# Performance work log

Hardware: AMD Instinct MI355X
Metric: run time of the kernel (lower is better)

Reference implementation:

```python
import jax, jax.numpy as jnp
import numpy as np

RATIO = 4   # compression ratio (group size)
H = 6       # index heads
D = 64      # index head dim = max(8, 768//6//2)
TOPK = 8    # index_topk
EPS = 1e-6  # rms_norm eps


def rms_norm(x):
    return x * jax.lax.rsqrt(jnp.mean(jnp.square(x), axis=-1, keepdims=True) + EPS)


def setup_inputs() -> dict:
    key = jax.random.key(0)
    k1, k2, k3, k4, k5 = jax.random.split(key, 5)
    B, T, E = 4, 4096, 768
    s = 0.02
    return {
        "x": jax.random.normal(k1, (B, T, E), jnp.float32),
        "wq": jax.random.normal(k2, (E, H * D), jnp.float32) * s,
        "wk": jax.random.normal(k3, (E, H * D), jnp.float32) * s,
        "wg": jax.random.normal(k4, (E, H * D), jnp.float32) * s,
        "ape": jax.random.normal(k5, (RATIO, H, D), jnp.float32) * s,
    }


def reference(x, wq, wk, wg, ape):
    B, T, E = x.shape
    G = -(-T // RATIO)          # ceil(T / ratio)
    pad = G * RATIO - T

    # --- compress keys: gated pooling over ratio-groups ---
    k = (x @ wk).reshape(B, T, H, D)
    gate = (x @ wg).reshape(B, T, H, D)
    if pad:
        k = jnp.pad(k, ((0, 0), (0, pad), (0, 0), (0, 0)))
        gate = jnp.pad(gate, ((0, 0), (0, pad), (0, 0), (0, 0)), constant_values=-jnp.inf)
    k = k.reshape(B, G, RATIO, H, D)
    gate = gate.reshape(B, G, RATIO, H, D) + ape[None, None]
    w = jax.nn.softmax(gate.astype(jnp.float32), axis=2).astype(k.dtype)
    keys = rms_norm(jnp.sum(k * w, axis=2))           # [B,G,H,D]
    group_ends = jnp.minimum(jnp.arange(RATIO - 1, G * RATIO, RATIO), T - 1)  # [G]

    # --- query-key scores ---
    q = rms_norm((x @ wq).reshape(B, T, H, D))
    scores = jnp.einsum('bthd,bghd->bhtg', q, keys) * (D ** -0.5)
    scores = jnp.mean(scores, axis=1)                 # [B,T,G]

    # --- causal mask over group ends, then top-k selection ---
    causal = group_ends[None, None, :] <= jnp.arange(T)[None, :, None]  # [1,T,G]
    scores = jnp.where(causal, scores, -jnp.inf)
    topk = min(TOPK, G)
    _, sel = jax.lax.top_k(scores, topk)              # [B,T,topk]

    # scatter selected indices into boolean mask
    bi = jnp.arange(B)[:, None, None]
    ti = jnp.arange(T)[None, :, None]
    mask = jnp.zeros((B, T, G), dtype=bool).at[bi, ti, sel].set(True)
    return (mask & causal, group_ends)
```

## Files before the change

### kernel.cpp

```cpp
#include <hip/hip_runtime.h>
#include <hip/hip_bf16.h>
#include <math.h>

#define B_    4
#define T_    4096
#define E_    768
#define H_    6
#define D_    64
#define HD_   384
#define G_    1024
#define RATIO_ 4
#define TOPK_ 8
#define MT_   (B_*T_)
#define NS_   1152

typedef __attribute__((ext_vector_type(8))) short short8;
typedef __attribute__((ext_vector_type(4))) float f32x4;
typedef __hip_bfloat16 bf16;

#define GLD16(g, l) __builtin_amdgcn_global_load_lds( \
    (const __attribute__((address_space(1))) void*)(g), \
    (__attribute__((address_space(3))) void*)(l), 16, 0, 0)

static __device__ __forceinline__ unsigned short f2bf(float f) {
  bf16 h = __float2bfloat16(f);
  return __builtin_bit_cast(unsigned short, h);
}
static __device__ __forceinline__ unsigned umax_(unsigned a, unsigned b) { return a > b ? a : b; }
static __device__ __forceinline__ unsigned umin_(unsigned a, unsigned b) { return a > b ? b : a; }

__global__ __launch_bounds__(256) void cvt_x_kernel(
    const float* __restrict__ in, bf16* __restrict__ out)
{
  size_t i = (size_t)blockIdx.x * 256 + threadIdx.x;
  const float4* p = reinterpret_cast<const float4*>(in) + i * 2;
  float4 v0 = p[0], v1 = p[1];
  float f[8] = {v0.x, v0.y, v0.z, v0.w, v1.x, v1.y, v1.z, v1.w};
  union { unsigned short u[8]; short8 v; } r;
#pragma unroll
  for (int k = 0; k < 8; ++k) r.u[k] = f2bf(f[k]);
  *reinterpret_cast<short8*>(out + i * 8) = r.v;
}

__global__ __launch_bounds__(256) void cvt_w_t(
    const float* __restrict__ wq, const float* __restrict__ wk,
    const float* __restrict__ wg, bf16* __restrict__ outbase)
{
  const int z = blockIdx.z;
  const float* src = z == 0 ? wq : (z == 1 ? wk : wg);
  __shared__ float t[32][33];
  int r = threadIdx.x >> 5, c = threadIdx.x & 31;
  int k0 = blockIdx.x * 32, n0 = blockIdx.y * 32;
#pragma unroll
  for (int i = 0; i < 4; ++i)
    t[r + i * 8][c] = src[(size_t)(k0 + r + i * 8) * HD_ + n0 + c];
  __syncthreads();
#pragma unroll
  for (int i = 0; i < 4; ++i) {
    int cc = n0 + r + i * 8;
    int ro = (z == 0) ? cc : 384 + ((cc >> 4) << 5) + ((z - 1) << 4) + (cc & 15);
    outbase[(size_t)ro * E_ + k0 + c] = __float2bfloat16(t[c][r + i * 8]);
  }
}

__global__ __launch_bounds__(256, 3) void gemm_qkg_mfma(
    const bf16* __restrict__ X, const bf16* __restrict__ Ws,
    const float* __restrict__ ape, bf16* __restrict__ Q,
    bf16* __restrict__ keys)
{
  __shared__ bf16 lds[2][8192];
  const int tid = threadIdx.x;
  const int lane = tid & 63, wv = tid >> 6;
  const int ll = lane & 15, lh = lane >> 4;
  const int m0 = blockIdx.x * 128, n0 = blockIdx.y * 128;
  const int srow = tid >> 3;
  const int sslot = (((tid & 7) ^ ((tid >> 3) & 7)) << 3);
  const bf16* pS = Ws + (size_t)(n0 + srow) * E_ + sslot;
  const bf16* pA0 = X + (size_t)(m0 + wv * 32 + ll) * E_ + lh * 8;
  const bf16* pA1 = pA0 + (size_t)16 * E_;

#define STAGE(b, k0) do { \
    char* base_ = (char*)&lds[b][0] + tid * 16; \
    GLD16(pS + (k0),            base_); \
    GLD16(pS + 32 * E_ + (k0),  base_ + 4096); \
    GLD16(pS + 64 * E_ + (k0),  base_ + 8192); \
    GLD16(pS + 96 * E_ + (k0),  base_ + 12288); \
  } while (0)
#define LOAD_A(dst, k0) do { \
    dst[0][0] = *reinterpret_cast<const short8*>(pA0 + (k0)); \
    dst[0][1] = *reinterpret_cast<const short8*>(pA0 + (k0) + 32); \
    dst[1][0] = *reinterpret_cast<const short8*>(pA1 + (k0)); \
    dst[1][1] = *reinterpret_cast<const short8*>(pA1 + (k0) + 32); \
  } while (0)

  f32x4 acc[2][8];
#pragma unroll
  for (int m = 0; m < 2; ++m)
#pragma unroll
    for (int n = 0; n < 8; ++n) acc[m][n] = (f32x4){0.f, 0.f, 0.f, 0.f};

  short8 curA[2][2], nxtA[2][2];
  LOAD_A(curA, 0);
  STAGE(0, 0);
#pragma unroll
  for (int m = 0; m < 2; ++m)
#pragma unroll
    for (int s = 0; s < 2; ++s) nxtA[m][s] = curA[m][s];

#pragma unroll
  for (int k = 0; k < 12; ++k) {
    const int k0 = k * 64;
    if (k < 11) {
      LOAD_A(nxtA, k0 + 64);
      STAGE((k + 1) & 1, k0 + 64);
    }
    if (k < 11) asm volatile("s_waitcnt vmcnt(8)" ::: "memory");
    else        asm volatile("s_waitcnt vmcnt(0)" ::: "memory");
    __builtin_amdgcn_s_barrier();
    __builtin_amdgcn_sched_barrier(0);
    const bf16* Lb = &lds[k & 1][0];
    short8 b0[8];
#pragma unroll
    for (int n = 0; n < 8; ++n)
      b0[n] = *reinterpret_cast<const short8*>(
          &Lb[(n * 16 + ll) * 64 + ((lh ^ (ll & 7)) << 3)]);
    asm volatile("s_waitcnt lgkmcnt(0)" ::: "memory");
    __builtin_amdgcn_sched_barrier(0);
#pragma unroll
    for (int m = 0; m < 2; ++m)
#pragma unroll
      for (int n = 0; n < 8; ++n)
        acc[m][n] = __builtin_amdgcn_mfma_f32_16x16x32_bf16(curA[m][0], b0[n], acc[m][n], 0, 0, 0);
    short8 b1[8];
#pragma unroll
    for (int n = 0; n < 8; ++n)
      b1[n] = *reinterpret_cast<const short8*>(
          &Lb[(n * 16 + ll) * 64 + (((4 + lh) ^ (ll & 7)) << 3)]);
    asm volatile("s_waitcnt lgkmcnt(0)" ::: "memory");
    __builtin_amdgcn_sched_barrier(0);
    __builtin_amdgcn_s_barrier();
#pragma unroll
    for (int m = 0; m < 2; ++m)
#pragma unroll
      for (int n = 0; n < 8; ++n)
        acc[m][n] = __builtin_amdgcn_mfma_f32_16x16x32_bf16(curA[m][1], b1[n], acc[m][n], 0, 0, 0);
#pragma unroll
    for (int m = 0; m < 2; ++m)
#pragma unroll
      for (int s = 0; s < 2; ++s) curA[m][s] = nxtA[m][s];
  }
#undef STAGE
#undef LOAD_A

  if (blockIdx.y < 3) {
#pragma unroll
    for (int m = 0; m < 2; ++m)
#pragma unroll
      for (int j = 0; j < 4; ++j) {
        int row = m0 + wv * 32 + m * 16 + lh * 4 + j;
#pragma unroll
        for (int h = 0; h < 2; ++h) {
          float ss = 0.f;
#pragma unroll
          for (int n = 4 * h; n < 4 * h + 4; ++n) ss += acc[m][n][j] * acc[m][n][j];
          ss += __shfl_xor(ss, 1, 64); ss += __shfl_xor(ss, 2, 64);
          ss += __shfl_xor(ss, 4, 64); ss += __shfl_xor(ss, 8, 64);
          float scl = rsqrtf(ss * (1.0f / D_) + 1e-6f);
#pragma unroll
          for (int n = 4 * h; n < 4 * h + 4; ++n)
            Q[(size_t)row * HD_ + n0 + n * 16 + ll] =
                __float2bfloat16(acc[m][n][j] * scl);
        }
      }
  } else {
    const int hcb = (n0 - 384) >> 1;
    float apev[4][4];
#pragma unroll
    for (int p = 0; p < 4; ++p) {
      int hc = hcb + p * 16 + ll;
#pragma unroll
      for (int j = 0; j < 4; ++j) apev[p][j] = ape[j * HD_ + hc];
    }
#pragma unroll
    for (int m = 0; m < 2; ++m) {
      float pooled[4];
#pragma unroll
      for (int p = 0; p < 4; ++p) {
        float g0 = acc[m][2 * p + 1][0] + apev[p][0];
        float g1 = acc[m][2 * p + 1][1] + apev[p][1];
        float g2 = acc[m][2 * p + 1][2] + apev[p][2];
        float g3 = acc[m][2 * p + 1][3] + apev[p][3];
        float mx = fmaxf(fmaxf(g0, g1), fmaxf(g2, g3));
        float e0 = expf(g0 - mx), e1 = expf(g1 - mx);
        float e2 = expf(g2 - mx), e3 = expf(g3 - mx);
        float inv = 1.0f / (e0 + e1 + e2 + e3);
        pooled[p] = (acc[m][2 * p][0] * e0 + acc[m][2 * p][1] * e1 +
                     acc[m][2 * p][2] * e2 + acc[m][2 * p][3] * e3) * inv;
      }
      float ss = pooled[0] * pooled[0] + pooled[1] * pooled[1] +
                 pooled[2] * pooled[2] + pooled[3] * pooled[3];
      ss += __shfl_xor(ss, 1, 64); ss += __shfl_xor(ss, 2, 64);
      ss += __shfl_xor(ss, 4, 64); ss += __shfl_xor(ss, 8, 64);
      float scl = rsqrtf(ss * (1.0f / D_) + 1e-6f);
      int prow = (m0 >> 2) + wv * 8 + m * 4 + lh;
#pragma unroll
      for (int p = 0; p < 4; ++p)
        keys[(size_t)prow * HD_ + hcb + p * 16 + ll] =
            __float2bfloat16(pooled[p] * scl);
    }
  }
}

#define CEx(a, bb) { unsigned h_ = umax_(a, bb), l_ = umin_(a, bb); a = h_; bb = l_; }
#define MERGE4() \
  _Pragma("unroll") \
  for (int st = 0; st < 2; ++st) { \
    const int off = 16 << st; \
    unsigned p0 = (unsigned)__shfl_xor((int)v0, off, 64); \
    unsigned p1 = (unsigned)__shfl_xor((int)v1, off, 64); \
    unsigned p2 = (unsigned)__shfl_xor((int)v2, off, 64); \
    unsigned p3 = (unsigned)__shfl_xor((int)v3, off, 64); \
    unsigned p4 = (unsigned)__shfl_xor((int)v4, off, 64); \
    unsigned p5 = (unsigned)__shfl_xor((int)v5, off, 64); \
    unsigned p6 = (unsigned)__shfl_xor((int)v6, off, 64); \
    unsigned p7 = (unsigned)__shfl_xor((int)v7, off, 64); \
    unsigned w0 = umax_(v0, p7), w1 = umax_(v1, p6); \
    unsigned w2 = umax_(v2, p5), w3 = umax_(v3, p4); \
    unsigned w4 = umax_(v4, p3), w5 = umax_(v5, p2); \
    unsigned w6 = umax_(v6, p1), w7 = umax_(v7, p0); \
    CEx(w0, w4); CEx(w1, w5); CEx(w2, w6); CEx(w3, w7); \
    CEx(w0, w2); CEx(w1, w3); CEx(w4, w6); CEx(w5, w7); \
    CEx(w0, w1); CEx(w2, w3); CEx(w4, w5); CEx(w6, w7); \
    v0 = w0; v1 = w1; v2 = w2; v3 = w3; v4 = w4; v5 = w5; v6 = w6; v7 = w7; \
  }

__global__ __launch_bounds__(128, 2) void score_topk8(
    const bf16* __restrict__ Qall, const bf16* __restrict__ Kall,
    int* __restrict__ mask, int* __restrict__ ends)
{
  __shared__ bf16 kbuf[2][12288];
  const int x = blockIdx.x;
  const int b = blockIdx.y;
  const int s = (b < 2) ? x : 127 - x;
  const int R0 = s << 5;
  const int tid = threadIdx.x;
  const int w = tid >> 6;
  const int lane = tid & 63;
  const int ll = lane & 15, lh = lane >> 4;

  if (x == 0 && b == 0) {
    int g = tid;
#pragma unroll
    for (int c = 0; c < 8; ++c, g += 128) {
      int e = (g << 2) + 3;
      ends[g] = e < T_ - 1 ? e : T_ - 1;
    }
  }

  int* mbase = mask + ((size_t)b * T_ + R0) * G_;
  {
    int4* m4 = reinterpret_cast<int4*>(mbase);
    const int4 z = make_int4(0, 0, 0, 0);
#pragma unroll
    for (int i = 0; i < 64; ++i) m4[i * 128 + tid] = z;
  }

  const bf16* Qb = Qall + (size_t)b * T_ * HD_;
  const bf16* Kb = Kall + (size_t)b * G_ * HD_;
  const int t = R0 + 16 * w + ll;
  const int gmax = (t + 1) >> 2;
  const int ntw = ((((R0 + 16 * w) >> 2) + 4) + 31) >> 5;
  const int nt  = ((((R0 + 16) >> 2) + 4) + 31) >> 5;

  const bf16* ksrc[12];
  int sdst[12];
#pragma unroll
  for (int i = 0; i < 12; ++i) {
    int u = (12 * w + i) * 64 + lane;
    int r = u / 48, sp = u - r * 48;
    int sl = sp ^ (r & 7);
    ksrc[i] = Kb + (size_t)r * HD_ + sl * 8;
    sdst[i] = u * 16;
  }
  short8 qf[12];
  {
    const bf16* pQ = Qb + (size_t)t * HD_ + lh * 8;
#pragma unroll
    for (int k = 0; k < 12; ++k)
      qf[k] = *reinterpret_cast<const short8*>(pQ + k * 32);
  }

#define KSTAGE(bf, g0) do { \
    char* bb_ = (char*)&kbuf[bf][0]; \
    _Pragma("unroll") \
    for (int i = 0; i < 12; ++i) \
      GLD16(ksrc[i] + (size_t)(g0) * HD_, bb_ + sdst[i]); \
  } while (0)

  unsigned v0 = 0, v1 = 0, v2 = 0, v3 = 0, v4 = 0, v5 = 0, v6 = 0, v7 = 0;
#define INS(xx) do { unsigned k_ = (xx), t_; \
    t_ = umax_(v0, k_); k_ = umin_(v0, k_); v0 = t_; \
    t_ = umax_(v1, k_); k_ = umin_(v1, k_); v1 = t_; \
    t_ = umax_(v2, k_); k_ = umin_(v2, k_); v2 = t_; \
    t_ = umax_(v3, k_); k_ = umin_(v3, k_); v3 = t_; \
    t_ = umax_(v4, k_); k_ = umin_(v4, k_); v4 = t_; \
    t_ = umax_(v5, k_); k_ = umin_(v5, k_); v5 = t_; \
    t_ = umax_(v6, k_); k_ = umin_(v6, k_); v6 = t_; \
    t_ = umax_(v7, k_); k_ = umin_(v7, k_); v7 = t_; } while (0)

  KSTAGE(0, 0);
  for (int mg = 0; mg < nt; ++mg) {
    if (mg + 1 < nt) {
      KSTAGE((mg + 1) & 1, (mg + 1) * 32);
      asm volatile("s_waitcnt vmcnt(12)" ::: "memory");
    } else {
      asm volatile("s_waitcnt vmcnt(0)" ::: "memory");
    }
    __builtin_amdgcn_s_barrier();
    __builtin_amdgcn_sched_barrier(0);
    if (mg < ntw) {
      const char* Lb = (const char*)&kbuf[mg & 1][0];
      f32x4 acc0 = (f32x4){0.f, 0.f, 0.f, 0.f};
      f32x4 acc1 = (f32x4){0.f, 0.f, 0.f, 0.f};
#pragma unroll
      for (int kk = 0; kk < 12; ++kk) {
        int sl = 4 * kk + lh;
        short8 k0 = *reinterpret_cast<const short8*>(
            Lb + (size_t)ll * 768 + ((sl ^ (ll & 7)) << 4));
        short8 k1 = *reinterpret_cast<const short8*>(
            Lb + (size_t)(16 + ll) * 768 + ((sl ^ (ll & 7)) << 4));
        acc0 = __builtin_amdgcn_mfma_f32_16x16x32_bf16(k0, qf[kk], acc0, 0, 0, 0);
        acc1 = __builtin_amdgcn_mfma_f32_16x16x32_bf16(k1, qf[kk], acc1, 0, 0, 0);
      }
      const int g0 = mg * 32;
#pragma unroll
      for (int j = 0; j < 4; ++j) {
        int g = g0 + lh * 4 + j;
        float xv = acc0[j] + 512.0f;
        unsigned key = (g < gmax)
            ? ((__builtin_bit_cast(unsigned, xv) & 0xFFFFFC00u) |
               (unsigned)(1023 - g))
            : 0u;
        INS(key);
      }
#pragma unroll
      for (int j = 0; j < 4; ++j) {
        int g = g0 + 16 + lh * 4 + j;
        float xv = acc1[j] + 512.0f;
        unsigned key = (g < gmax)
            ? ((__builtin_bit_cast(unsigned, xv) & 0xFFFFFC00u) |
               (unsigned)(1023 - g))
            : 0u;
        INS(key);
      }
    }
    __builtin_amdgcn_s_barrier();
  }
#undef INS
#undef KSTAGE

  MERGE4();

  __syncthreads();
  if (lh == 0) {
    int* rb = mbase + (size_t)(16 * w + ll) * G_;
    if (v0) rb[1023 - (v0 & 1023)] = 1;
    if (v1) rb[1023 - (v1 & 1023)] = 1;
    if (v2) rb[1023 - (v2 & 1023)] = 1;
    if (v3) rb[1023 - (v3 & 1023)] = 1;
    if (v4) rb[1023 - (v4 & 1023)] = 1;
    if (v5) rb[1023 - (v5 & 1023)] = 1;
    if (v6) rb[1023 - (v6 & 1023)] = 1;
    if (v7) rb[1023 - (v7 & 1023)] = 1;
  }
}

extern "C" void kernel_launch(void* const* d_in, const int* in_sizes, int n_in,
                              void* d_out, int out_size, void* d_ws, size_t ws_size,
                              hipStream_t stream)
{
  const float* x   = (const float*)d_in[0];
  const float* wq  = (const float*)d_in[1];
  const float* wk  = (const float*)d_in[2];
  const float* wg  = (const float*)d_in[3];
  const float* ape = (const float*)d_in[4];

  bf16* Ws   = (bf16*)d_ws;
  bf16* qb   = Ws + (size_t)NS_ * E_;
  bf16* keys = qb + (size_t)MT_ * HD_;

  bf16* xb = (bf16*)d_out;

  cvt_x_kernel<<<dim3(MT_ * E_ / 8 / 256), dim3(256), 0, stream>>>(x, xb);
  cvt_w_t<<<dim3(E_ / 32, HD_ / 32, 3), dim3(256), 0, stream>>>(wq, wk, wg, Ws);

  gemm_qkg_mfma<<<dim3(MT_ / 128, NS_ / 128), dim3(256), 0, stream>>>(
      xb, Ws, ape, qb, keys);

  score_topk8<<<dim3(128, B_), dim3(128), 0, stream>>>(
      qb, keys, (int*)d_out, (int*)d_out + (size_t)B_ * T_ * G_);
}
```

Before: 105.7 us.

## Fuse fp32-to-bf16 conversion of x into GEMM A-operand loads

Removes the separate cvt_x kernel and its bf16 copy of x, so the GEMM reads fp32 x directly and converts it to bf16 in registers before the MFMAs. This drops one full pass over x (write plus re-read) and a launch, and the vmcnt wait is adjusted for the doubled load count. In exchange, each of the 9 N-column blocks now reads twice as many bytes of A, and the extra registers for the fp32 prefetch may pressure occupancy at 3 blocks per CU.

```diff
diff --git a/kernel.cpp b/kernel.cpp
--- a/kernel.cpp
+++ b/kernel.cpp
@@ -26,21 +26,14 @@
   bf16 h = __float2bfloat16(f);
   return __builtin_bit_cast(unsigned short, h);
 }
+static __device__ __forceinline__ short8 cvt8(float4 a, float4 b) {
+  union { unsigned short u[8]; short8 v; } r;
+  r.u[0] = f2bf(a.x); r.u[1] = f2bf(a.y); r.u[2] = f2bf(a.z); r.u[3] = f2bf(a.w);
+  r.u[4] = f2bf(b.x); r.u[5] = f2bf(b.y); r.u[6] = f2bf(b.z); r.u[7] = f2bf(b.w);
+  return r.v;
+}
 static __device__ __forceinline__ unsigned umax_(unsigned a, unsigned b) { return a > b ? a : b; }
 static __device__ __forceinline__ unsigned umin_(unsigned a, unsigned b) { return a > b ? b : a; }
-
-__global__ __launch_bounds__(256) void cvt_x_kernel(
-    const float* __restrict__ in, bf16* __restrict__ out)
-{
-  size_t i = (size_t)blockIdx.x * 256 + threadIdx.x;
-  const float4* p = reinterpret_cast<const float4*>(in) + i * 2;
-  float4 v0 = p[0], v1 = p[1];
-  float f[8] = {v0.x, v0.y, v0.z, v0.w, v1.x, v1.y, v1.z, v1.w};
-  union { unsigned short u[8]; short8 v; } r;
-#pragma unroll
-  for (int k = 0; k < 8; ++k) r.u[k] = f2bf(f[k]);
-  *reinterpret_cast<short8*>(out + i * 8) = r.v;
-}
 
 __global__ __launch_bounds__(256) void cvt_w_t(
     const float* __restrict__ wq, const float* __restrict__ wk,
@@ -64,7 +57,7 @@
 }
 
 __global__ __launch_bounds__(256, 3) void gemm_qkg_mfma(
-    const bf16* __restrict__ X, const bf16* __restrict__ Ws,
+    const float* __restrict__ Xf, const bf16* __restrict__ Ws,
     const float* __restrict__ ape, bf16* __restrict__ Q,
     bf16* __restrict__ keys)
 {
@@ -76,8 +69,8 @@
   const int srow = tid >> 3;
   const int sslot = (((tid & 7) ^ ((tid >> 3) & 7)) << 3);
   const bf16* pS = Ws + (size_t)(n0 + srow) * E_ + sslot;
-  const bf16* pA0 = X + (size_t)(m0 + wv * 32 + ll) * E_ + lh * 8;
-  const bf16* pA1 = pA0 + (size_t)16 * E_;
+  const float* pA0 = Xf + (size_t)(m0 + wv * 32 + ll) * E_ + lh * 8;
+  const float* pA1 = pA0 + (size_t)16 * E_;
 
 #define STAGE(b, k0) do { \
     char* base_ = (char*)&lds[b][0] + tid * 16; \
@@ -86,11 +79,15 @@
     GLD16(pS + 64 * E_ + (k0),  base_ + 8192); \
     GLD16(pS + 96 * E_ + (k0),  base_ + 12288); \
   } while (0)
-#define LOAD_A(dst, k0) do { \
-    dst[0][0] = *reinterpret_cast<const short8*>(pA0 + (k0)); \
-    dst[0][1] = *reinterpret_cast<const short8*>(pA0 + (k0) + 32); \
-    dst[1][0] = *reinterpret_cast<const short8*>(pA1 + (k0)); \
-    dst[1][1] = *reinterpret_cast<const short8*>(pA1 + (k0) + 32); \
+#define LOAD_AF(dst, k0) do { \
+    dst[0][0][0] = *reinterpret_cast<const float4*>(pA0 + (k0)); \
+    dst[0][0][1] = *reinterpret_cast<const float4*>(pA0 + (k0) + 4); \
+    dst[0][1][0] = *reinterpret_cast<const float4*>(pA0 + (k0) + 32); \
+    dst[0][1][1] = *reinterpret_cast<const float4*>(pA0 + (k0) + 36); \
+    dst[1][0][0] = *reinterpret_cast<const float4*>(pA1 + (k0)); \
+    dst[1][0][1] = *reinterpret_cast<const float4*>(pA1 + (k0) + 4); \
+    dst[1][1][0] = *reinterpret_cast<const float4*>(pA1 + (k0) + 32); \
+    dst[1][1][1] = *reinterpret_cast<const float4*>(pA1 + (k0) + 36); \
   } while (0)
 
   f32x4 acc[2][8];
@@ -99,22 +96,24 @@
 #pragma unroll
     for (int n = 0; n < 8; ++n) acc[m][n] = (f32x4){0.f, 0.f, 0.f, 0.f};
 
-  short8 curA[2][2], nxtA[2][2];
-  LOAD_A(curA, 0);
+  float4 nxtF[2][2][2];
+  short8 curA[2][2];
+  LOAD_AF(nxtF, 0);
   STAGE(0, 0);
 #pragma unroll
   for (int m = 0; m < 2; ++m)
 #pragma unroll
-    for (int s = 0; s < 2; ++s) nxtA[m][s] = curA[m][s];
+    for (int s = 0; s < 2; ++s)
+      curA[m][s] = cvt8(nxtF[m][s][0], nxtF[m][s][1]);
 
 #pragma unroll
   for (int k = 0; k < 12; ++k) {
     const int k0 = k * 64;
     if (k < 11) {
-      LOAD_A(nxtA, k0 + 64);
+      LOAD_AF(nxtF, k0 + 64);
       STAGE((k + 1) & 1, k0 + 64);
     }
-    if (k < 11) asm volatile("s_waitcnt vmcnt(8)" ::: "memory");
+    if (k < 11) asm volatile("s_waitcnt vmcnt(12)" ::: "memory");
     else        asm volatile("s_waitcnt vmcnt(0)" ::: "memory");
     __builtin_amdgcn_s_barrier();
     __builtin_amdgcn_sched_barrier(0);
@@ -144,13 +143,16 @@
 #pragma unroll
       for (int n = 0; n < 8; ++n)
         acc[m][n] = __builtin_amdgcn_mfma_f32_16x16x32_bf16(curA[m][1], b1[n], acc[m][n], 0, 0, 0);
-#pragma unroll
-    for (int m = 0; m < 2; ++m)
-#pragma unroll
-      for (int s = 0; s < 2; ++s) curA[m][s] = nxtA[m][s];
+    if (k < 11) {
+#pragma unroll
+      for (int m = 0; m < 2; ++m)
+#pragma unroll
+        for (int s = 0; s < 2; ++s)
+          curA[m][s] = cvt8(nxtF[m][s][0], nxtF[m][s][1]);
+    }
   }
 #undef STAGE
-#undef LOAD_A
+#undef LOAD_AF
 
   if (blockIdx.y < 3) {
 #pragma unroll
@@ -389,13 +391,10 @@
   bf16* qb   = Ws + (size_t)NS_ * E_;
   bf16* keys = qb + (size_t)MT_ * HD_;
 
-  bf16* xb = (bf16*)d_out;
-
-  cvt_x_kernel<<<dim3(MT_ * E_ / 8 / 256), dim3(256), 0, stream>>>(x, xb);
   cvt_w_t<<<dim3(E_ / 32, HD_ / 32, 3), dim3(256), 0, stream>>>(wq, wk, wg, Ws);
 
   gemm_qkg_mfma<<<dim3(MT_ / 128, NS_ / 128), dim3(256), 0, stream>>>(
-      xb, Ws, ape, qb, keys);
+      x, Ws, ape, qb, keys);
 
   score_topk8<<<dim3(128, B_), dim3(128), 0, stream>>>(
       qb, keys, (int*)d_out, (int*)d_out + (size_t)B_ * T_ * G_);
```

Measured after the change: 129.5 us. 22.4% more time.
